# Performance work log

Measured on AMD Instinct MI355X. Metric: run time of the kernel, lower is better.

The kernel has to match this reference:

```python
import jax, jax.numpy as jnp
import numpy as np

DIM = 64
N_EMBED = 1024


def setup_inputs() -> dict:
    key = jax.random.key(0)
    k1, k2 = jax.random.split(key)
    input = jax.random.normal(k1, (32, 64, 64, DIM), dtype=jnp.float32)
    embed = jax.random.normal(k2, (DIM, N_EMBED), dtype=jnp.float32)
    return {"input": input, "embed": embed}


def reference(input, embed):
    # Flatten all leading dims: [N, dim]
    flatten = input.reshape(-1, DIM)
    # Squared L2 distance to each code: [N, n_embed]
    dist = (
        jnp.sum(flatten * flatten, axis=1, keepdims=True)
        - 2.0 * (flatten @ embed)
        + jnp.sum(embed * embed, axis=0, keepdims=True)
    )
    embed_ind_flat = jnp.argmin(dist, axis=1)  # argmax(-dist)
    embed_ind = embed_ind_flat.reshape(input.shape[:-1])
    # Codebook lookup: embed.T is [n_embed, dim]
    quantize = jnp.take(embed.T, embed_ind, axis=0)  # [..., dim]
    # Commitment loss with detached quantize
    diff = jnp.mean((jax.lax.stop_gradient(quantize) - input) ** 2)
    # Straight-through estimator
    quantize = input + jax.lax.stop_gradient(quantize - input)
    num_used_codebooks = -1  # eval-mode constant, as in the torch module
    return quantize, diff, embed_ind, num_used_codebooks
```

## Files before the change

### kernel.cpp

```cpp
#include <hip/hip_runtime.h>
#include <hip/hip_bf16.h>

#define DIM      64
#define NCODE    1024
#define NROWS    131072
#define NTILES   64
#define TAU      0.006f
#define TSTRIDE  4160

typedef __attribute__((ext_vector_type(8))) short  short8;
typedef __attribute__((ext_vector_type(4))) float  f32x4;

#define DIFF_OFF 8388608
#define IND_OFF  8388609
#define NU_OFF   (8388609 + 131072)

#define WS_HEE      0
#define WS_EMBEDT   1024
#define WS_PARTIALS 66560
#define WS_PIDX     67072
#define WS_COUNTER  198144
#define WS_FLAGLIST 198145
#define WS_BPK      329220

__device__ __forceinline__ unsigned short bf16rn(float f) {
    unsigned int u = __float_as_uint(f);
    return (unsigned short)((u + 0x7FFFu + ((u >> 16) & 1u)) >> 16);
}
__device__ __forceinline__ float bf16tof(unsigned short h) {
    return __uint_as_float(((unsigned int)h) << 16);
}
__device__ __forceinline__ unsigned umin_(unsigned a, unsigned b) { return a < b ? a : b; }
__device__ __forceinline__ unsigned umax_(unsigned a, unsigned b) { return a > b ? a : b; }

__global__ __launch_bounds__(256) void vq_prep(const float* __restrict__ embed,
                                               float* __restrict__ embedT,
                                               float* __restrict__ hee,
                                               int* __restrict__ counter,
                                               unsigned char* __restrict__ bpk) {
    if (blockIdx.x < 4) {
        int c = blockIdx.x * 256 + threadIdx.x;
        if (c == 0) *counter = 0;
        float s = 0.f;
#pragma unroll
        for (int d = 0; d < DIM; ++d) {
            float v = embed[d * NCODE + c];
            embedT[c * DIM + d] = v;
            s = fmaf(v, v, s);
        }
        hee[c] = 0.5f * s;
    } else {
        int t  = (blockIdx.x - 4) * 256 + threadIdx.x;
        int s  = t & 1;
        int l  = (t >> 1) & 63;
        int ct = t >> 7;
        int c  = ct * 16 + (l & 15);
        int kb = s * 32 + (l >> 4) * 8;

        unsigned int hw[4], lw[4];
#pragma unroll
        for (int w = 0; w < 4; ++w) {
            float v0 = embed[(kb + 2 * w)     * NCODE + c];
            float v1 = embed[(kb + 2 * w + 1) * NCODE + c];
            unsigned short h0 = bf16rn(v0), h1 = bf16rn(v1);
            unsigned short l0 = bf16rn(v0 - bf16tof(h0));
            unsigned short l1 = bf16rn(v1 - bf16tof(h1));
            hw[w] = (unsigned int)h0 | ((unsigned int)h1 << 16);
            lw[w] = (unsigned int)l0 | ((unsigned int)l1 << 16);
        }
        uint4* dst_h = (uint4*)(bpk + ct * TSTRIDE + 64 + s * 1024 + l * 16);
        uint4* dst_l = (uint4*)(bpk + ct * TSTRIDE + 64 + s * 1024 + l * 16 + 2048);
        *dst_h = make_uint4(hw[0], hw[1], hw[2], hw[3]);
        *dst_l = make_uint4(lw[0], lw[1], lw[2], lw[3]);
        if (s == 0 && l < 16) {
            float ss = 0.f;
#pragma unroll
            for (int d = 0; d < DIM; ++d) {
                float v = embed[d * NCODE + c];
                ss = fmaf(v, v, ss);
            }
            *(float*)(bpk + ct * TSTRIDE + l * 4) = 0.5f * ss;
        }
    }
}

#define ISSUE_T(C0, C1, C2, C3, HH, FA, HA)                                   \
    asm volatile("global_load_dwordx4 %0, %1, off"             : "=v"(C0) : "v"(FA)); \
    asm volatile("global_load_dwordx4 %0, %1, off offset:1024" : "=v"(C1) : "v"(FA)); \
    asm volatile("global_load_dwordx4 %0, %1, off offset:2048" : "=v"(C2) : "v"(FA)); \
    asm volatile("global_load_dwordx4 %0, %1, off offset:3072" : "=v"(C3) : "v"(FA)); \
    asm volatile("global_load_dword %0, %1, off"               : "=v"(HH) : "v"(HA));

#define WAITN(N)                                                              \
    asm volatile("s_waitcnt vmcnt(" #N ")" ::: "memory");                     \
    __builtin_amdgcn_sched_barrier(0);

__global__ __launch_bounds__(256, 4) void vq_score_mfma(const float* __restrict__ input,
                                                        const unsigned char* __restrict__ bpk,
                                                        float* __restrict__ pidx,
                                                        int* __restrict__ counter,
                                                        int* __restrict__ flaglist) {
    const int tid   = threadIdx.x;
    const int wid   = tid >> 6;
    const int lane  = tid & 63;
    const int g     = lane >> 4;
    const int lc    = lane & 15;
    const int rbase = (blockIdx.x * 4 + wid) * 32;

    short8 ah[2][2], al[2][2];
    float  hx[2][4];
#pragma unroll
    for (int m = 0; m < 2; ++m) {
        float ssum = 0.f;
#pragma unroll
        for (int s = 0; s < 2; ++s) {
            const float* xr = input + (size_t)(rbase + m * 16 + lc) * DIM + s * 32 + g * 8;
            float4 f0 = *(const float4*)(xr);
            float4 f1 = *(const float4*)(xr + 4);
            float xf[8] = {f0.x, f0.y, f0.z, f0.w, f1.x, f1.y, f1.z, f1.w};
            short8 h8, l8;
#pragma unroll
            for (int j = 0; j < 8; ++j) {
                ssum = fmaf(xf[j], xf[j], ssum);
                float nx = -xf[j];
                unsigned short hb = bf16rn(nx);
                h8[j] = (short)hb;
                l8[j] = (short)bf16rn(nx - bf16tof(hb));
            }
            ah[m][s] = h8;
            al[m][s] = l8;
        }
        ssum += __shfl_xor(ssum, 16, 64);
        ssum += __shfl_xor(ssum, 32, 64);
#pragma unroll
        for (int j = 0; j < 4; ++j)
            hx[m][j] = 0.5f * __shfl(ssum, g * 4 + j, 64) + 1.0f;
    }

    unsigned m1[8], m2[8];
#pragma unroll
    for (int t = 0; t < 8; ++t) { m1[t] = 0xFFFFFFFFu; m2[t] = 0xFFFFFFFFu; }

#define COMPT(T, C0, C1, C2, C3, HH)                                          \
    {   short8 s0 = __builtin_bit_cast(short8, C0);                           \
        short8 s1 = __builtin_bit_cast(short8, C1);                           \
        short8 s2 = __builtin_bit_cast(short8, C2);                           \
        short8 s3 = __builtin_bit_cast(short8, C3);                           \
        _Pragma("unroll")                                                     \
        for (int m = 0; m < 2; ++m) {                                         \
            f32x4 acc = {(HH) + hx[m][0], (HH) + hx[m][1],                    \
                         (HH) + hx[m][2], (HH) + hx[m][3]};                   \
            acc = __builtin_amdgcn_mfma_f32_16x16x32_bf16(ah[m][0], s0, acc, 0, 0, 0); \
            acc = __builtin_amdgcn_mfma_f32_16x16x32_bf16(al[m][0], s0, acc, 0, 0, 0); \
            acc = __builtin_amdgcn_mfma_f32_16x16x32_bf16(ah[m][0], s2, acc, 0, 0, 0); \
            acc = __builtin_amdgcn_mfma_f32_16x16x32_bf16(ah[m][1], s1, acc, 0, 0, 0); \
            acc = __builtin_amdgcn_mfma_f32_16x16x32_bf16(al[m][1], s1, acc, 0, 0, 0); \
            acc = __builtin_amdgcn_mfma_f32_16x16x32_bf16(ah[m][1], s3, acc, 0, 0, 0); \
            _Pragma("unroll")                                                 \
            for (int j = 0; j < 4; ++j) {                                     \
                unsigned bits = __float_as_uint(acc[j]);                      \
                unsigned pk   = (bits & 0xFFFFFFC0u) | (unsigned)(T);         \
                int s = m * 4 + j;                                            \
                m2[s] = umin_(m2[s], umax_(pk, m1[s]));                       \
                m1[s] = umin_(m1[s], pk);                                     \
            }                                                                 \
        } }

    unsigned long long fA = (unsigned long long)(uintptr_t)(bpk + 64 + lane * 16);
    unsigned long long hA = (unsigned long long)(uintptr_t)(bpk + lc * 4);
    unsigned long long fB = fA + TSTRIDE;
    unsigned long long hB = hA + TSTRIDE;

    uint4 a0, a1, a2, a3;  float ahh;
    uint4 b0, b1, b2, b3;  float bhh;

    ISSUE_T(a0, a1, a2, a3, ahh, fA, hA);
    fA += 2 * TSTRIDE;  hA += 2 * TSTRIDE;

    for (int ct = 0; ct < NTILES - 2; ct += 2) {
        ISSUE_T(b0, b1, b2, b3, bhh, fB, hB);
        fB += 2 * TSTRIDE;  hB += 2 * TSTRIDE;
        WAITN(5);
        COMPT(ct, a0, a1, a2, a3, ahh);
        ISSUE_T(a0, a1, a2, a3, ahh, fA, hA);
        fA += 2 * TSTRIDE;  hA += 2 * TSTRIDE;
        WAITN(5);
        COMPT(ct + 1, b0, b1, b2, b3, bhh);
    }
    ISSUE_T(b0, b1, b2, b3, bhh, fB, hB);
    WAITN(5);
    COMPT(NTILES - 2, a0, a1, a2, a3, ahh);
    WAITN(0);
    COMPT(NTILES - 1, b0, b1, b2, b3, bhh);

#undef COMPT

#pragma unroll
    for (int m = 0; m < 2; ++m) {
#pragma unroll
        for (int j = 0; j < 4; ++j) {
            int s = m * 4 + j;
            unsigned v1 = m1[s], v2 = m2[s];
            int ii = (int)(((v1 & 63u) << 4) | (unsigned)lc);
#pragma unroll
            for (int d = 1; d < 16; d <<= 1) {
                unsigned o1 = __shfl_xor(v1, d, 64);
                int      oi = __shfl_xor(ii, d, 64);
                unsigned o2 = __shfl_xor(v2, d, 64);
                bool sw = (o1 < v1) || (o1 == v1 && oi < ii);
                unsigned losing = sw ? v1 : o1;
                v2 = umin_(umin_(v2, o2), losing);
                v1 = sw ? o1 : v1;
                ii = sw ? oi : ii;
            }
            if (lc == 0) {
                int r = rbase + m * 16 + g * 4 + j;
                pidx[r] = (float)ii;
                float gap = __uint_as_float(v2 & 0xFFFFFFC0u)
                          - __uint_as_float(v1 & 0xFFFFFFC0u);
                if (gap < TAU) {
                    int p = atomicAdd(counter, 1);
                    flaglist[p] = r;
                }
            }
        }
    }
}

__global__ __launch_bounds__(64) void vq_rescore(const float* __restrict__ input,
                                                 const float* __restrict__ embedT,
                                                 const float* __restrict__ hee,
                                                 const int* __restrict__ counter,
                                                 const int* __restrict__ flaglist,
                                                 float* __restrict__ pidx) {
    const int lane = threadIdx.x;
    const int cnt  = *counter;
    for (int i = blockIdx.x * 2; i < cnt; i += gridDim.x * 2) {
        const int r0 = flaglist[i];
        const int r1 = (i + 1 < cnt) ? flaglist[i + 1] : r0;
        float4 xa[16], xb[16];
        {
            const float4* pa = (const float4*)(input + (size_t)r0 * DIM);
            const float4* pb = (const float4*)(input + (size_t)r1 * DIM);
#pragma unroll
            for (int k = 0; k < 16; ++k) { xa[k] = pa[k]; xb[k] = pb[k]; }
        }
        float bestA = -3.402823466e+38f, bestB = -3.402823466e+38f;
        int   biA = 0, biB = 0;
#pragma unroll 1
        for (int k = 0; k < 16; ++k) {
            int c = lane * 16 + k;
            const float4* e4 = (const float4*)(embedT + (size_t)c * DIM);
            float hh = hee[c];
            float a0 = -hh, a1 = 0.f, a2 = 0.f, a3 = 0.f;
            float b0 = -hh, b1 = 0.f, b2 = 0.f, b3 = 0.f;
#pragma unroll
            for (int q = 0; q < 4; ++q) {
                float4 e0 = e4[4 * q + 0], e1 = e4[4 * q + 1];
                float4 e2 = e4[4 * q + 2], e3 = e4[4 * q + 3];
                float4 p0 = xa[4 * q + 0], p1 = xa[4 * q + 1];
                float4 p2 = xa[4 * q + 2], p3 = xa[4 * q + 3];
                float4 q0 = xb[4 * q + 0], q1 = xb[4 * q + 1];
                float4 q2 = xb[4 * q + 2], q3 = xb[4 * q + 3];
                a0 = fmaf(e0.x, p0.x, a0); a0 = fmaf(e0.y, p0.y, a0);
                a0 = fmaf(e0.z, p0.z, a0); a0 = fmaf(e0.w, p0.w, a0);
                a1 = fmaf(e1.x, p1.x, a1); a1 = fmaf(e1.y, p1.y, a1);
                a1 = fmaf(e1.z, p1.z, a1); a1 = fmaf(e1.w, p1.w, a1);
                a2 = fmaf(e2.x, p2.x, a2); a2 = fmaf(e2.y, p2.y, a2);
                a2 = fmaf(e2.z, p2.z, a2); a2 = fmaf(e2.w, p2.w, a2);
                a3 = fmaf(e3.x, p3.x, a3); a3 = fmaf(e3.y, p3.y, a3);
                a3 = fmaf(e3.z, p3.z, a3); a3 = fmaf(e3.w, p3.w, a3);
                b0 = fmaf(e0.x, q0.x, b0); b0 = fmaf(e0.y, q0.y, b0);
                b0 = fmaf(e0.z, q0.z, b0); b0 = fmaf(e0.w, q0.w, b0);
                b1 = fmaf(e1.x, q1.x, b1); b1 = fmaf(e1.y, q1.y, b1);
                b1 = fmaf(e1.z, q1.z, b1); b1 = fmaf(e1.w, q1.w, b1);
                b2 = fmaf(e2.x, q2.x, b2); b2 = fmaf(e2.y, q2.y, b2);
                b2 = fmaf(e2.z, q2.z, b2); b2 = fmaf(e2.w, q2.w, b2);
                b3 = fmaf(e3.x, q3.x, b3); b3 = fmaf(e3.y, q3.y, b3);
                b3 = fmaf(e3.z, q3.z, b3); b3 = fmaf(e3.w, q3.w, b3);
            }
            float sA = (a0 + a1) + (a2 + a3);
            float sB = (b0 + b1) + (b2 + b3);
            if (sA > bestA) { bestA = sA; biA = c; }
            if (sB > bestB) { bestB = sB; biB = c; }
        }
#pragma unroll
        for (int d = 1; d < 64; d <<= 1) {
            float oA = __shfl_xor(bestA, d, 64);
            int   iA = __shfl_xor(biA, d, 64);
            bool  sA = (oA > bestA) || (oA == bestA && iA < biA);
            bestA = sA ? oA : bestA;
            biA   = sA ? iA : biA;
            float oB = __shfl_xor(bestB, d, 64);
            int   iB = __shfl_xor(biB, d, 64);
            bool  sB = (oB > bestB) || (oB == bestB && iB < biB);
            bestB = sB ? oB : bestB;
            biB   = sB ? iB : biB;
        }
        if (lane == 0) {
            pidx[r0] = (float)biA;
            pidx[r1] = (float)biB;
        }
    }
}

__global__ __launch_bounds__(256) void vq_combine(const float* __restrict__ input,
                                                  const float* __restrict__ embedT,
                                                  const float* __restrict__ pidx,
                                                  float* __restrict__ out_q,
                                                  float* __restrict__ out_ind,
                                                  float* __restrict__ partials) {
    __shared__ float wsum[4];
    const int tid = threadIdx.x;
    const int r   = blockIdx.x * 256 + tid;

    int bi = (int)pidx[r];
    out_ind[r] = (float)bi;

    float acc = 0.f;
    {
        const float4* x4 = (const float4*)(input + (size_t)r * DIM);
        const float4* q4 = (const float4*)(embedT + (size_t)bi * DIM);
        float4* o4 = (float4*)(out_q + (size_t)r * DIM);
#pragma unroll
        for (int k = 0; k < 16; ++k) {
            float4 q = q4[k];
            float4 x = x4[k];
            o4[k] = q;
            float dx = q.x - x.x; acc = fmaf(dx, dx, acc);
            dx = q.y - x.y;       acc = fmaf(dx, dx, acc);
            dx = q.z - x.z;       acc = fmaf(dx, dx, acc);
            dx = q.w - x.w;       acc = fmaf(dx, dx, acc);
        }
    }
#pragma unroll
    for (int off = 32; off > 0; off >>= 1) acc += __shfl_down(acc, off, 64);
    if ((tid & 63) == 0) wsum[tid >> 6] = acc;
    __syncthreads();
    if (tid == 0) partials[blockIdx.x] = (wsum[0] + wsum[1]) + (wsum[2] + wsum[3]);
}

__global__ __launch_bounds__(256) void vq_finalize(const float* __restrict__ partials,
                                                   float* __restrict__ out,
                                                   int out_size) {
    __shared__ float sm[256];
    int t = threadIdx.x;
    float v = partials[t] + partials[t + 256];
    sm[t] = v;
    __syncthreads();
    for (int s = 128; s > 0; s >>= 1) {
        if (t < s) sm[t] += sm[t + s];
        __syncthreads();
    }
    if (t == 0) out[DIFF_OFF] = sm[0] / 8388608.0f;
    if (t == 1 && out_size > NU_OFF) out[NU_OFF] = -1.0f;
}

extern "C" void kernel_launch(void* const* d_in, const int* in_sizes, int n_in,
                              void* d_out, int out_size, void* d_ws, size_t ws_size,
                              hipStream_t stream) {
    const float* input = (const float*)d_in[0];
    const float* embed = (const float*)d_in[1];
    float* out = (float*)d_out;
    float* ws  = (float*)d_ws;

    float* hee      = ws + WS_HEE;
    float* embedT   = ws + WS_EMBEDT;
    float* partials = ws + WS_PARTIALS;
    float* pidx     = ws + WS_PIDX;
    int*   counter  = (int*)(ws + WS_COUNTER);
    int*   flaglist = (int*)(ws + WS_FLAGLIST);
    unsigned char* bpk = (unsigned char*)(ws + WS_BPK);

    vq_prep<<<36, 256, 0, stream>>>(embed, embedT, hee, counter, bpk);
    vq_score_mfma<<<1024, 256, 0, stream>>>(input, bpk, pidx, counter, flaglist);
    vq_rescore<<<2048, 64, 0, stream>>>(input, embedT, hee, counter, flaglist, pidx);
    vq_combine<<<512, 256, 0, stream>>>(input, embedT, pidx,
                                        out, out + IND_OFF, partials);
    vq_finalize<<<1, 256, 0, stream>>>(partials, out, out_size);
}
```

Before: 110.3 us.

## Fuse codebook gather and per-row MSE into scoring kernel, drop combine pass

```diff
diff --git a/kernel.cpp b/kernel.cpp
--- a/kernel.cpp
+++ b/kernel.cpp
@@ -18,7 +18,7 @@
 #define WS_HEE      0
 #define WS_EMBEDT   1024
 #define WS_PARTIALS 66560
-#define WS_PIDX     67072
+#define WS_RMSE     67072
 #define WS_COUNTER  198144
 #define WS_FLAGLIST 198145
 #define WS_BPK      329220
@@ -97,9 +97,14 @@
 
 __global__ __launch_bounds__(256, 4) void vq_score_mfma(const float* __restrict__ input,
                                                         const unsigned char* __restrict__ bpk,
-                                                        float* __restrict__ pidx,
+                                                        const float* __restrict__ embedT,
+                                                        float* __restrict__ out_q,
+                                                        float* __restrict__ out_ind,
+                                                        float* __restrict__ row_mse,
                                                         int* __restrict__ counter,
                                                         int* __restrict__ flaglist) {
+    __shared__ int scode[4][32];
+
     const int tid   = threadIdx.x;
     const int wid   = tid >> 6;
     const int lane  = tid & 63;
@@ -150,12 +155,14 @@
         for (int m = 0; m < 2; ++m) {                                         \
             f32x4 acc = {(HH) + hx[m][0], (HH) + hx[m][1],                    \
                          (HH) + hx[m][2], (HH) + hx[m][3]};                   \
+            __builtin_amdgcn_s_setprio(1);                                    \
             acc = __builtin_amdgcn_mfma_f32_16x16x32_bf16(ah[m][0], s0, acc, 0, 0, 0); \
             acc = __builtin_amdgcn_mfma_f32_16x16x32_bf16(al[m][0], s0, acc, 0, 0, 0); \
             acc = __builtin_amdgcn_mfma_f32_16x16x32_bf16(ah[m][0], s2, acc, 0, 0, 0); \
             acc = __builtin_amdgcn_mfma_f32_16x16x32_bf16(ah[m][1], s1, acc, 0, 0, 0); \
             acc = __builtin_amdgcn_mfma_f32_16x16x32_bf16(al[m][1], s1, acc, 0, 0, 0); \
             acc = __builtin_amdgcn_mfma_f32_16x16x32_bf16(ah[m][1], s3, acc, 0, 0, 0); \
+            __builtin_amdgcn_s_setprio(0);                                    \
             _Pragma("unroll")                                                 \
             for (int j = 0; j < 4; ++j) {                                     \
                 unsigned bits = __float_as_uint(acc[j]);                      \
@@ -214,8 +221,11 @@
                 ii = sw ? oi : ii;
             }
             if (lc == 0) {
-                int r = rbase + m * 16 + g * 4 + j;
-                pidx[r] = (float)ii;
+                int rr = m * 16 + g * 4 + j;
+                int r  = rbase + rr;
+                scode[wid][rr] = ii;
+                out_ind[r] = (float)ii;
+                row_mse[r] = 2.0f * (__uint_as_float(v1 & 0xFFFFFFC0u) - 1.0f);
                 float gap = __uint_as_float(v2 & 0xFFFFFFC0u)
                           - __uint_as_float(v1 & 0xFFFFFFC0u);
                 if (gap < TAU) {
@@ -225,6 +235,16 @@
             }
         }
     }
+
+    __syncthreads();
+    {
+        int r2   = lane >> 1;
+        int code = scode[wid][r2];
+        const float4* src = (const float4*)(embedT + (size_t)code * DIM) + (lane & 1) * 8;
+        float4*       dst = (float4*)(out_q + (size_t)(rbase + r2) * DIM) + (lane & 1) * 8;
+#pragma unroll
+        for (int k = 0; k < 8; ++k) dst[k] = src[k];
+    }
 }
 
 __global__ __launch_bounds__(64) void vq_rescore(const float* __restrict__ input,
@@ -232,18 +252,27 @@
                                                  const float* __restrict__ hee,
                                                  const int* __restrict__ counter,
                                                  const int* __restrict__ flaglist,
-                                                 float* __restrict__ pidx) {
+                                                 float* __restrict__ out_q,
+                                                 float* __restrict__ out_ind,
+                                                 float* __restrict__ row_mse) {
     const int lane = threadIdx.x;
     const int cnt  = *counter;
     for (int i = blockIdx.x * 2; i < cnt; i += gridDim.x * 2) {
         const int r0 = flaglist[i];
         const int r1 = (i + 1 < cnt) ? flaglist[i + 1] : r0;
         float4 xa[16], xb[16];
+        float ssA = 0.f, ssB = 0.f;
         {
             const float4* pa = (const float4*)(input + (size_t)r0 * DIM);
             const float4* pb = (const float4*)(input + (size_t)r1 * DIM);
 #pragma unroll
-            for (int k = 0; k < 16; ++k) { xa[k] = pa[k]; xb[k] = pb[k]; }
+            for (int k = 0; k < 16; ++k) {
+                xa[k] = pa[k]; xb[k] = pb[k];
+                ssA = fmaf(xa[k].x, xa[k].x, ssA); ssA = fmaf(xa[k].y, xa[k].y, ssA);
+                ssA = fmaf(xa[k].z, xa[k].z, ssA); ssA = fmaf(xa[k].w, xa[k].w, ssA);
+                ssB = fmaf(xb[k].x, xb[k].x, ssB); ssB = fmaf(xb[k].y, xb[k].y, ssB);
+                ssB = fmaf(xb[k].z, xb[k].z, ssB); ssB = fmaf(xb[k].w, xb[k].w, ssB);
+            }
         }
         float bestA = -3.402823466e+38f, bestB = -3.402823466e+38f;
         int   biA = 0, biB = 0;
@@ -298,41 +327,30 @@
             biB   = sB ? iB : biB;
         }
         if (lane == 0) {
-            pidx[r0] = (float)biA;
-            pidx[r1] = (float)biB;
-        }
-    }
-}
-
-__global__ __launch_bounds__(256) void vq_combine(const float* __restrict__ input,
-                                                  const float* __restrict__ embedT,
-                                                  const float* __restrict__ pidx,
-                                                  float* __restrict__ out_q,
-                                                  float* __restrict__ out_ind,
-                                                  float* __restrict__ partials) {
+            out_ind[r0] = (float)biA;
+            row_mse[r0] = ssA - 2.0f * bestA;
+            out_ind[r1] = (float)biB;
+            row_mse[r1] = ssB - 2.0f * bestB;
+        }
+        {
+            int half = lane >> 4;
+            int fi   = lane & 15;
+            if (half == 0) {
+                ((float4*)(out_q + (size_t)r0 * DIM))[fi] =
+                    ((const float4*)(embedT + (size_t)biA * DIM))[fi];
+            } else if (half == 1) {
+                ((float4*)(out_q + (size_t)r1 * DIM))[fi] =
+                    ((const float4*)(embedT + (size_t)biB * DIM))[fi];
+            }
+        }
+    }
+}
+
+__global__ __launch_bounds__(256) void vq_mse_reduce(const float* __restrict__ row_mse,
+                                                     float* __restrict__ partials) {
     __shared__ float wsum[4];
     const int tid = threadIdx.x;
-    const int r   = blockIdx.x * 256 + tid;
-
-    int bi = (int)pidx[r];
-    out_ind[r] = (float)bi;
-
-    float acc = 0.f;
-    {
-        const float4* x4 = (const float4*)(input + (size_t)r * DIM);
-        const float4* q4 = (const float4*)(embedT + (size_t)bi * DIM);
-        float4* o4 = (float4*)(out_q + (size_t)r * DIM);
-#pragma unroll
-        for (int k = 0; k < 16; ++k) {
-            float4 q = q4[k];
-            float4 x = x4[k];
-            o4[k] = q;
-            float dx = q.x - x.x; acc = fmaf(dx, dx, acc);
-            dx = q.y - x.y;       acc = fmaf(dx, dx, acc);
-            dx = q.z - x.z;       acc = fmaf(dx, dx, acc);
-            dx = q.w - x.w;       acc = fmaf(dx, dx, acc);
-        }
-    }
+    float acc = row_mse[blockIdx.x * 256 + tid];
 #pragma unroll
     for (int off = 32; off > 0; off >>= 1) acc += __shfl_down(acc, off, 64);
     if ((tid & 63) == 0) wsum[tid >> 6] = acc;
@@ -367,15 +385,17 @@
     float* hee      = ws + WS_HEE;
     float* embedT   = ws + WS_EMBEDT;
     float* partials = ws + WS_PARTIALS;
-    float* pidx     = ws + WS_PIDX;
+    float* row_mse  = ws + WS_RMSE;
     int*   counter  = (int*)(ws + WS_COUNTER);
     int*   flaglist = (int*)(ws + WS_FLAGLIST);
     unsigned char* bpk = (unsigned char*)(ws + WS_BPK);
 
     vq_prep<<<36, 256, 0, stream>>>(embed, embedT, hee, counter, bpk);
-    vq_score_mfma<<<1024, 256, 0, stream>>>(input, bpk, pidx, counter, flaglist);
-    vq_rescore<<<2048, 64, 0, stream>>>(input, embedT, hee, counter, flaglist, pidx);
-    vq_combine<<<512, 256, 0, stream>>>(input, embedT, pidx,
-                                        out, out + IND_OFF, partials);
+    vq_score_mfma<<<1024, 256, 0, stream>>>(input, bpk, embedT,
+                                            out, out + IND_OFF, row_mse,
+                                            counter, flaglist);
+    vq_rescore<<<2048, 64, 0, stream>>>(input, embedT, hee, counter, flaglist,
+                                        out, out + IND_OFF, row_mse);
+    vq_mse_reduce<<<512, 256, 0, stream>>>(row_mse, partials);
     vq_finalize<<<1, 256, 0, stream>>>(partials, out, out_size);
 }
```

Measured after the change: 98.46 us. -10.7%, faster.
